# Performance work log

Measured on AMD Instinct MI355X. Metric: run time of the kernel, lower is better.

Reference implementation:

```python
import jax, jax.numpy as jnp
import numpy as np

N_HEAD = 16

def setup_inputs() -> dict:
    key = jax.random.key(0)
    ks = jax.random.split(key, 9)
    H = 2048
    def w(k, shape, scale=0.02):
        return jax.random.normal(k, shape, dtype=jnp.float32) * scale
    return {
        'h':  jax.random.normal(ks[0], (4, 2048, H), dtype=jnp.float32),
        'Wq': w(ks[1], (H, H)), 'bq': w(ks[2], (H,)),
        'Wk': w(ks[3], (H, H)), 'bk': w(ks[4], (H,)),
        'Wv': w(ks[5], (H, H)), 'bv': w(ks[6], (H,)),
        'Wo': w(ks[7], (H, H)), 'bo': w(ks[8], (H,)),
    }

def reference(h, Wq, bq, Wk, bk, Wv, bv, Wo, bo):
    B, S, H = h.shape
    nh = N_HEAD
    hd = H // nh
    # QKV projections (torch Linear: x @ W.T + b)
    q = (h @ Wq.T + bq).reshape(B, S, nh, hd)
    k = (h @ Wk.T + bk).reshape(B, S, nh, hd)
    v = (h @ Wv.T + bv).reshape(B, S, nh, hd)
    scale = 1.0 / jnp.sqrt(jnp.float32(hd))
    # causal attention scores [B, nh, S, S]
    scores = jnp.einsum('bqhd,bkhd->bhqk', q, k) * scale
    causal = jnp.tril(jnp.ones((S, S), dtype=bool))
    scores = jnp.where(causal, scores, jnp.finfo(scores.dtype).min)
    attn = jax.nn.softmax(scores, axis=-1)
    o = jnp.einsum('bhqk,bkhd->bqhd', attn, v).reshape(B, S, H)
    return o @ Wo.T + bo
```

## Files before the change

kernel.cpp:

```cpp
#include <hip/hip_runtime.h>
#include <hip/hip_bf16.h>
#include <math.h>


using bf16x8 = __attribute__((ext_vector_type(8))) __bf16;
using f32x4  = __attribute__((ext_vector_type(4))) float;
using s16x8  = __attribute__((ext_vector_type(8))) short;

#define MFMA16(a, b, c) __builtin_amdgcn_mfma_f32_16x16x32_bf16((a), (b), (c), 0, 0, 0)

__device__ __forceinline__ unsigned short f2bf(float f) {
  unsigned u = __float_as_uint(f);
  u += 0x7FFFu + ((u >> 16) & 1u);
  return (unsigned short)(u >> 16);
}

__device__ __forceinline__ void gload16(const void* g, void* l) {
  __builtin_amdgcn_global_load_lds((const __attribute__((address_space(1))) void*)g,
                                   (__attribute__((address_space(3))) void*)l,
                                   16, 0, 0);
}

__global__ void cvt_kernel(const float* __restrict__ in, unsigned short* __restrict__ out, int n4) {
  int i = blockIdx.x * 256 + threadIdx.x;
  if (i >= n4) return;
  float4 v = ((const float4*)in)[i];
  ushort4 o;
  o.x = f2bf(v.x); o.y = f2bf(v.y); o.z = f2bf(v.z); o.w = f2bf(v.w);
  ((ushort4*)out)[i] = o;
}


#define GEMM_PRE()                                                             \
  const int tid = threadIdx.x;                                                 \
  const int wave = tid >> 6, lane = tid & 63;                                  \
  const int lo = lane & 15, hi = lane >> 4;                                    \
  const int wr = wave >> 2, wc = wave & 3;                                     \
  const int r4 = lane >> 2, s4 = lane & 3;                                     \
  const int scol = ((s4 ^ (r4 & 3)) << 3);                                     \
  const unsigned short* aS[2]; const unsigned short* bS[2];                    \
  _Pragma("unroll")                                                            \
  for (int j = 0; j < 2; ++j) {                                                \
    aS[j] = A + (size_t)(m0 + (wave * 2 + j) * 16 + r4) * 2048 + scol;         \
    bS[j] = W + (size_t)(n0 + (wave * 2 + j) * 16 + r4) * 2048 + scol;         \
  }                                                                            \
  f32x4 acc[8][4] = {};

#define STAGE2(BUF, J)                                                         \
  do {                                                                         \
    gload16(aS[J], &lA[BUF][(wave * 2 + (J)) * 512]);                          \
    gload16(bS[J], &lB[BUF][(wave * 2 + (J)) * 512]);                          \
    aS[J] += 32; bS[J] += 32;                                                  \
  } while (0)

#define LDA4_(dst, MH, BUF)                                                    \
  do {                                                                         \
    _Pragma("unroll")                                                          \
    for (int im = 0; im < 4; ++im)                                             \
      dst[im] = *(const bf16x8*)&lA[BUF][(wr * 128 + (MH)*64 + im * 16 + lo) * 32 + \
                                         ((hi ^ (lo & 3)) << 3)];              \
  } while (0)

#define LDB4_(dst, BUF)                                                        \
  do {                                                                         \
    _Pragma("unroll")                                                          \
    for (int ni = 0; ni < 4; ++ni)                                             \
      dst[ni] = *(const bf16x8*)&lB[BUF][(wc * 64 + ni * 16 + lo) * 32 +       \
                                         ((hi ^ (lo & 3)) << 3)];              \
  } while (0)

#define MF16(MH, aF, bF)                                                       \
  do {                                                                         \
    __builtin_amdgcn_s_setprio(1);                                             \
    _Pragma("unroll")                                                          \
    for (int im = 0; im < 4; ++im)                                             \
      _Pragma("unroll")                                                        \
      for (int ni = 0; ni < 4; ++ni)                                           \
        acc[(MH)*4 + im][ni] = MFMA16(aF[im], bF[ni], acc[(MH)*4 + im][ni]);   \
    __builtin_amdgcn_s_setprio(0);                                             \
  } while (0)

#define BAR __builtin_amdgcn_s_barrier()
#define VMC(N) asm volatile("s_waitcnt vmcnt(" #N ")" ::: "memory")

#define TILE(RBUF, SBUF, COND, VN)                                             \
  do {                                                                         \
    bf16x8 aF[4], aG[4], bF[4];                                                \
    LDA4_(aF, 0, RBUF); LDB4_(bF, RBUF);                                       \
    if (COND) STAGE2(SBUF, 0);                                                 \
    BAR; MF16(0, aF, bF); BAR;                                                 \
    LDA4_(aG, 1, RBUF);                                                        \
    if (COND) STAGE2(SBUF, 1);                                                 \
    BAR; MF16(1, aG, bF); VMC(VN); BAR;                                        \
  } while (0)

#define GEMM_MAIN()                                                            \
  STAGE2(0, 0); STAGE2(0, 1); STAGE2(1, 0); STAGE2(1, 1);                      \
  STAGE2(2, 0); STAGE2(2, 1);                                                  \
  VMC(8); BAR;                                                                 \
  for (int u = 0; u < 15; ++u) {                                               \
    TILE(0, 3, true, 8); TILE(1, 0, true, 8);                                  \
    TILE(2, 1, true, 8); TILE(3, 2, true, 8);                                  \
  }                                                                            \
              \
  TILE(0, 3, true, 8); TILE(1, 0, false, 4);                                   \
  TILE(2, 1, false, 0); TILE(3, 2, false, 0);

__global__ __launch_bounds__(512, 2)
void gemm_qkv(const unsigned short* __restrict__ A,
              const unsigned short* __restrict__ W,
              const float* __restrict__ bq, const float* __restrict__ bk,
              const float* __restrict__ bv,
              unsigned short* __restrict__ Q, unsigned short* __restrict__ Kq,
              unsigned short* __restrict__ V) {
  __shared__ unsigned short lA[4][256 * 32];
  __shared__ unsigned short lB[4][256 * 32];
  const int bid = blockIdx.x;
  const int sid = (bid & 7) * 96 + (bid >> 3);
  const int bm = sid / 24, bn = sid % 24;
  const int m0 = bm * 256, n0 = bn * 256;
  GEMM_PRE();
  GEMM_MAIN();

  const int which = n0 >> 11;
  const float* bias = (which == 0) ? bq : (which == 1) ? bk : bv;
  unsigned short* dst = (which == 0) ? Q : (which == 1) ? Kq : V;
#pragma unroll
  for (int mi = 0; mi < 8; mi++)
#pragma unroll
    for (int ni = 0; ni < 4; ni++) {
      int n_g = n0 + wc * 64 + ni * 16 + lo;
      int n2 = n_g & 2047;
      int head = n2 >> 7, d = n2 & 127;
      float bb = bias[n2];
#pragma unroll
      for (int i = 0; i < 4; i++) {
        int m = m0 + wr * 128 + mi * 16 + hi * 4 + i;
        int b = m >> 11, s = m & 2047;
        dst[(((size_t)b * 16 + head) * 2048 + s) * 128 + d] = f2bf(acc[mi][ni][i] + bb);
      }
    }
}

__global__ __launch_bounds__(512, 2)
void gemm_out(const unsigned short* __restrict__ A,
              const unsigned short* __restrict__ W,
              const float* __restrict__ bo, float* __restrict__ out) {
  __shared__ unsigned short lA[4][256 * 32];
  __shared__ unsigned short lB[4][256 * 32];
  const int bid = blockIdx.x;
  const int sid = (bid & 7) * 32 + (bid >> 3);
  const int bm = sid >> 3, bn = sid & 7;
  const int m0 = bm * 256, n0 = bn * 256;
  GEMM_PRE();
  GEMM_MAIN();

#pragma unroll
  for (int mi = 0; mi < 8; mi++)
#pragma unroll
    for (int ni = 0; ni < 4; ni++) {
      int n_g = n0 + wc * 64 + ni * 16 + lo;
      float bb = bo[n_g];
#pragma unroll
      for (int i = 0; i < 4; i++) {
        int m = m0 + wr * 128 + mi * 16 + hi * 4 + i;
        out[(size_t)m * 2048 + n_g] = acc[mi][ni][i] + bb;
      }
    }
}

__global__ __launch_bounds__(256, 2)
void attn_kernel(const unsigned short* __restrict__ Qb,
                 const unsigned short* __restrict__ Kb,
                 const unsigned short* __restrict__ Vb,
                 unsigned short* __restrict__ Ob) {
  __shared__ unsigned short lK[32 * 128];
  __shared__ unsigned short lVt[128 * 40];
  __shared__ unsigned short lP[4][32 * 40];

  const int tid = threadIdx.x;
  const int wave = tid >> 6, lane = tid & 63;
  const int lo = lane & 15, hi = lane >> 4;
  const int bh = blockIdx.x & 63;
  const int qt = 15 - (blockIdx.x >> 6);
  const int q0 = qt * 128 + wave * 32;
  const size_t base = (size_t)bh * 2048 * 128;
  const float scale = 0.08838834764831845f;

  bf16x8 aq[2][4];
#pragma unroll
  for (int mi = 0; mi < 2; mi++)
#pragma unroll
    for (int dk = 0; dk < 4; dk++)
      aq[mi][dk] = *(const bf16x8*)&Qb[base + (size_t)(q0 + mi * 16 + lo) * 128 + dk * 32 + hi * 8];

  f32x4 acc[2][8] = {};
  float mrun[2][4], lrun[2][4];
#pragma unroll
  for (int a = 0; a < 2; a++)
#pragma unroll
    for (int b = 0; b < 4; b++) { mrun[a][b] = -INFINITY; lrun[a][b] = 0.0f; }

  const int ktn = qt * 4 + 4;
  const int qmax_w = q0 + 31;

  for (int kt = 0; kt < ktn; kt++) {
    __syncthreads();
#pragma unroll
    for (int j = 0; j < 2; j++) {
      int c = wave * 2 + j;
      int row = c * 4 + hi;
      int srccol = (lo * 16) ^ ((row & 7) << 4);
      const unsigned short* g = Kb + base + (size_t)(kt * 32 + row) * 128 + (srccol >> 1);
      gload16(g, &lK[c * 512]);
    }
    {
      int rr = tid & 15;
      int c0 = (tid >> 4) * 8;
      const unsigned short* vp = Vb + base + (size_t)(kt * 32 + 2 * rr) * 128 + c0;
      s16x8 va = *(const s16x8*)vp;
      s16x8 vb2 = *(const s16x8*)(vp + 128);
#pragma unroll
      for (int j = 0; j < 8; j++)
        *(ushort2*)&lVt[(c0 + j) * 40 + 2 * rr] =
            make_ushort2((unsigned short)va[j], (unsigned short)vb2[j]);
    }
    __syncthreads();

    if (kt * 32 <= qmax_w) {
      f32x4 sc[2][2] = {};
#pragma unroll
      for (int ni = 0; ni < 2; ni++)
#pragma unroll
        for (int dk = 0; dk < 4; dk++) {
          int row = ni * 16 + lo;
          int col = (dk * 32 + hi * 8) ^ ((row & 7) << 3);
          bf16x8 bk_ = *(const bf16x8*)&lK[row * 128 + col];
          sc[0][ni] = MFMA16(aq[0][dk], bk_, sc[0][ni]);
          sc[1][ni] = MFMA16(aq[1][dk], bk_, sc[1][ni]);
        }

      unsigned short* lPw = &lP[wave][0];
#pragma unroll
      for (int mi = 0; mi < 2; mi++)
#pragma unroll
        for (int i = 0; i < 4; i++) {
          int qrow = q0 + mi * 16 + hi * 4 + i;
          float s0 = sc[mi][0][i] * scale;
          float s1 = sc[mi][1][i] * scale;
          int kc = kt * 32 + lo;
          if (kc > qrow) s0 = -INFINITY;
          if (kc + 16 > qrow) s1 = -INFINITY;
          float mt = fmaxf(s0, s1);
          mt = fmaxf(mt, __shfl_xor(mt, 1));
          mt = fmaxf(mt, __shfl_xor(mt, 2));
          mt = fmaxf(mt, __shfl_xor(mt, 4));
          mt = fmaxf(mt, __shfl_xor(mt, 8));
          float mo = mrun[mi][i];
          float mn = fmaxf(mo, mt);
          float alpha = __expf(mo - mn);
          float p0 = __expf(s0 - mn);
          float p1 = __expf(s1 - mn);
          float rs = p0 + p1;
          rs += __shfl_xor(rs, 1);
          rs += __shfl_xor(rs, 2);
          rs += __shfl_xor(rs, 4);
          rs += __shfl_xor(rs, 8);
          mrun[mi][i] = mn;
          lrun[mi][i] = lrun[mi][i] * alpha + rs;
#pragma unroll
          for (int ni = 0; ni < 8; ni++) acc[mi][ni][i] *= alpha;
          int prow = mi * 16 + hi * 4 + i;
          lPw[prow * 40 + lo] = f2bf(p0);
          lPw[prow * 40 + 16 + lo] = f2bf(p1);
        }

      bf16x8 ap0 = *(const bf16x8*)&lPw[(lo) * 40 + hi * 8];
      bf16x8 ap1 = *(const bf16x8*)&lPw[(16 + lo) * 40 + hi * 8];
#pragma unroll
      for (int ni = 0; ni < 8; ni++) {
        bf16x8 bv_ = *(const bf16x8*)&lVt[(ni * 16 + lo) * 40 + hi * 8];
        acc[0][ni] = MFMA16(ap0, bv_, acc[0][ni]);
        acc[1][ni] = MFMA16(ap1, bv_, acc[1][ni]);
      }
    }
  }

  const int b = bh >> 4, hh = bh & 15;
#pragma unroll
  for (int mi = 0; mi < 2; mi++)
#pragma unroll
    for (int i = 0; i < 4; i++) {
      float inv = 1.0f / lrun[mi][i];
      int s = q0 + mi * 16 + hi * 4 + i;
      size_t rowbase = ((size_t)b * 2048 + s) * 2048 + hh * 128 + lo;
#pragma unroll
      for (int ni = 0; ni < 8; ni++)
        Ob[rowbase + ni * 16] = f2bf(acc[mi][ni][i] * inv);
    }
}

extern "C" void kernel_launch(void* const* d_in, const int* in_sizes, int n_in,
                              void* d_out, int out_size, void* d_ws, size_t ws_size,
                              hipStream_t stream) {
  const float* h  = (const float*)d_in[0];
  const float* Wq = (const float*)d_in[1];
  const float* bq = (const float*)d_in[2];
  const float* Wk = (const float*)d_in[3];
  const float* bk = (const float*)d_in[4];
  const float* Wv = (const float*)d_in[5];
  const float* bv = (const float*)d_in[6];
  const float* Wo = (const float*)d_in[7];
  const float* bo = (const float*)d_in[8];
  float* out = (float*)d_out;

  char* ws = (char*)d_ws;
  unsigned short* h_bf  = (unsigned short*)(ws + 0);
  unsigned short* Qb    = (unsigned short*)(ws + 33554432);
  unsigned short* Kb    = (unsigned short*)(ws + 67108864);
  unsigned short* Vb    = (unsigned short*)(ws + 100663296);
  unsigned short* Wqkv  = (unsigned short*)(ws + 134217728);
  unsigned short* Wo_bf = (unsigned short*)(ws + 159383552);
  unsigned short* Ob    = h_bf;

  cvt_kernel<<<16384, 256, 0, stream>>>(h, h_bf, 4194304);
  cvt_kernel<<<4096, 256, 0, stream>>>(Wq, Wqkv, 1048576);
  cvt_kernel<<<4096, 256, 0, stream>>>(Wk, Wqkv + 4194304, 1048576);
  cvt_kernel<<<4096, 256, 0, stream>>>(Wv, Wqkv + 8388608, 1048576);
  cvt_kernel<<<4096, 256, 0, stream>>>(Wo, Wo_bf, 1048576);

  gemm_qkv<<<dim3(768), dim3(512), 0, stream>>>(h_bf, Wqkv, bq, bk, bv, Qb, Kb, Vb);

  attn_kernel<<<dim3(1024), dim3(256), 0, stream>>>(Qb, Kb, Vb, Ob);

  gemm_out<<<dim3(256), dim3(512), 0, stream>>>(Ob, Wo_bf, bo, out);
}
```

Before: 516.0 us.

## Lazy softmax rescaling, exp2 with folded scale, MFMA-based row sums in attention

Result: faster. 468.0 us (-9.3%).

```diff
diff --git a/kernel.cpp b/kernel.cpp
--- a/kernel.cpp
+++ b/kernel.cpp
@@ -102,7 +102,6 @@
     TILE(0, 3, true, 8); TILE(1, 0, true, 8);                                  \
     TILE(2, 1, true, 8); TILE(3, 2, true, 8);                                  \
   }                                                                            \
-              \
   TILE(0, 3, true, 8); TILE(1, 0, false, 4);                                   \
   TILE(2, 1, false, 0); TILE(3, 2, false, 0);
 
@@ -175,7 +174,7 @@
                  const unsigned short* __restrict__ Vb,
                  unsigned short* __restrict__ Ob) {
   __shared__ unsigned short lK[32 * 128];
-  __shared__ unsigned short lVt[128 * 40];
+  __shared__ unsigned short lVt[144 * 42];
   __shared__ unsigned short lP[4][32 * 40];
 
   const int tid = threadIdx.x;
@@ -185,7 +184,12 @@
   const int qt = 15 - (blockIdx.x >> 6);
   const int q0 = qt * 128 + wave * 32;
   const size_t base = (size_t)bh * 2048 * 128;
-  const float scale = 0.08838834764831845f;
+  const float SCL = 0.08838834764831845f * 1.4426950408889634f;
+  const float THR = 11.5416f;
+
+#pragma unroll
+  for (int x = tid; x < 512; x += 256)
+    lVt[(128 + (x >> 5)) * 42 + (x & 31)] = 0x3F80;
 
   bf16x8 aq[2][4];
 #pragma unroll
@@ -194,12 +198,12 @@
     for (int dk = 0; dk < 4; dk++)
       aq[mi][dk] = *(const bf16x8*)&Qb[base + (size_t)(q0 + mi * 16 + lo) * 128 + dk * 32 + hi * 8];
 
-  f32x4 acc[2][8] = {};
-  float mrun[2][4], lrun[2][4];
+  f32x4 acc[2][9] = {};
+  float mrun[2][4];
 #pragma unroll
   for (int a = 0; a < 2; a++)
 #pragma unroll
-    for (int b = 0; b < 4; b++) { mrun[a][b] = -INFINITY; lrun[a][b] = 0.0f; }
+    for (int b = 0; b < 4; b++) mrun[a][b] = -INFINITY;
 
   const int ktn = qt * 4 + 4;
   const int qmax_w = q0 + 31;
@@ -222,7 +226,7 @@
       s16x8 vb2 = *(const s16x8*)(vp + 128);
 #pragma unroll
       for (int j = 0; j < 8; j++)
-        *(ushort2*)&lVt[(c0 + j) * 40 + 2 * rr] =
+        *(ushort2*)&lVt[(c0 + j) * 42 + 2 * rr] =
             make_ushort2((unsigned short)va[j], (unsigned short)vb2[j]);
     }
     __syncthreads();
@@ -240,36 +244,49 @@
           sc[1][ni] = MFMA16(aq[1][dk], bk_, sc[1][ni]);
         }
 
-      unsigned short* lPw = &lP[wave][0];
+      float s0_[2][4], s1_[2][4];
+      bool cond = true;
 #pragma unroll
       for (int mi = 0; mi < 2; mi++)
 #pragma unroll
         for (int i = 0; i < 4; i++) {
           int qrow = q0 + mi * 16 + hi * 4 + i;
-          float s0 = sc[mi][0][i] * scale;
-          float s1 = sc[mi][1][i] * scale;
           int kc = kt * 32 + lo;
+          float s0 = sc[mi][0][i] * SCL;
+          float s1 = sc[mi][1][i] * SCL;
           if (kc > qrow) s0 = -INFINITY;
           if (kc + 16 > qrow) s1 = -INFINITY;
-          float mt = fmaxf(s0, s1);
-          mt = fmaxf(mt, __shfl_xor(mt, 1));
-          mt = fmaxf(mt, __shfl_xor(mt, 2));
-          mt = fmaxf(mt, __shfl_xor(mt, 4));
-          mt = fmaxf(mt, __shfl_xor(mt, 8));
-          float mo = mrun[mi][i];
-          float mn = fmaxf(mo, mt);
-          float alpha = __expf(mo - mn);
-          float p0 = __expf(s0 - mn);
-          float p1 = __expf(s1 - mn);
-          float rs = p0 + p1;
-          rs += __shfl_xor(rs, 1);
-          rs += __shfl_xor(rs, 2);
-          rs += __shfl_xor(rs, 4);
-          rs += __shfl_xor(rs, 8);
-          mrun[mi][i] = mn;
-          lrun[mi][i] = lrun[mi][i] * alpha + rs;
-#pragma unroll
-          for (int ni = 0; ni < 8; ni++) acc[mi][ni][i] *= alpha;
+          s0_[mi][i] = s0; s1_[mi][i] = s1;
+          cond = cond && (fmaxf(s0, s1) <= mrun[mi][i] + THR);
+        }
+
+      if (!__all((int)cond)) {
+#pragma unroll
+        for (int mi = 0; mi < 2; mi++)
+#pragma unroll
+          for (int i = 0; i < 4; i++) {
+            float mt = fmaxf(s0_[mi][i], s1_[mi][i]);
+            mt = fmaxf(mt, __shfl_xor(mt, 1));
+            mt = fmaxf(mt, __shfl_xor(mt, 2));
+            mt = fmaxf(mt, __shfl_xor(mt, 4));
+            mt = fmaxf(mt, __shfl_xor(mt, 8));
+            float mo = mrun[mi][i];
+            float mn = fmaxf(mo, mt);
+            float alpha = exp2f(mo - mn);
+            mrun[mi][i] = mn;
+#pragma unroll
+            for (int ni = 0; ni < 9; ni++) acc[mi][ni][i] *= alpha;
+          }
+      }
+
+      unsigned short* lPw = &lP[wave][0];
+#pragma unroll
+      for (int mi = 0; mi < 2; mi++)
+#pragma unroll
+        for (int i = 0; i < 4; i++) {
+          float m = mrun[mi][i];
+          float p0 = exp2f(s0_[mi][i] - m);
+          float p1 = exp2f(s1_[mi][i] - m);
           int prow = mi * 16 + hi * 4 + i;
           lPw[prow * 40 + lo] = f2bf(p0);
           lPw[prow * 40 + 16 + lo] = f2bf(p1);
@@ -278,8 +295,8 @@
       bf16x8 ap0 = *(const bf16x8*)&lPw[(lo) * 40 + hi * 8];
       bf16x8 ap1 = *(const bf16x8*)&lPw[(16 + lo) * 40 + hi * 8];
 #pragma unroll
-      for (int ni = 0; ni < 8; ni++) {
-        bf16x8 bv_ = *(const bf16x8*)&lVt[(ni * 16 + lo) * 40 + hi * 8];
+      for (int ni = 0; ni < 9; ni++) {
+        bf16x8 bv_ = *(const bf16x8*)&lVt[(ni * 16 + lo) * 42 + hi * 8];
         acc[0][ni] = MFMA16(ap0, bv_, acc[0][ni]);
         acc[1][ni] = MFMA16(ap1, bv_, acc[1][ni]);
       }
@@ -291,7 +308,7 @@
   for (int mi = 0; mi < 2; mi++)
 #pragma unroll
     for (int i = 0; i < 4; i++) {
-      float inv = 1.0f / lrun[mi][i];
+      float inv = 1.0f / acc[mi][8][i];
       int s = q0 + mi * 16 + hi * 4 + i;
       size_t rowbase = ((size_t)b * 2048 + s) * 2048 + hh * 128 + lo;
 #pragma unroll
```
